# Kernel tuning notes

Measured on AMD Instinct MI355X. Metric: run time of the kernel, lower is better.

The kernel has to match this reference:

```python
import jax, jax.numpy as jnp
import numpy as np

N_HEAD, D_MODEL, D_K, D_V = 8, 128, 16, 16
EPS = 1e-5


def entmax15(x):
    # 1.5-entmax along last axis (Peters & Martins 2019, exact sort-based algo)
    x = x * 0.5
    x = x - jnp.max(x, axis=-1, keepdims=True)
    xs = jnp.flip(jnp.sort(x, axis=-1), axis=-1)  # descending
    K = x.shape[-1]
    rho = jnp.arange(1, K + 1, dtype=x.dtype)
    mean = jnp.cumsum(xs, axis=-1) / rho
    mean_sq = jnp.cumsum(xs * xs, axis=-1) / rho
    delta = (1.0 - rho * (mean_sq - mean * mean)) / rho
    tau = mean - jnp.sqrt(jnp.clip(delta, 0.0))
    support = jnp.sum(tau <= xs, axis=-1, keepdims=True)  # support size k*
    tau_star = jnp.take_along_axis(tau, support - 1, axis=-1)
    p = jnp.clip(x - tau_star, 0.0)
    return p * p


def layer_norm(x, gamma, beta):
    mu = jnp.mean(x, axis=-1, keepdims=True)
    var = jnp.mean((x - mu) ** 2, axis=-1, keepdims=True)
    return gamma * (x - mu) * jax.lax.rsqrt(var + EPS) + beta


def setup_inputs() -> dict:
    key = jax.random.key(0)
    ks = jax.random.split(key, 24)
    B, Lq, Lk, D = 4, 1024, 2048, D_MODEL
    s = 0.05
    f = jax.random.normal
    return {
        "q": f(ks[0], (B, Lq, D), jnp.float32),
        "k": f(ks[1], (B, Lk, D), jnp.float32),
        "v": f(ks[2], (B, Lk, D), jnp.float32),
        "v_2": f(ks[3], (B, Lq, D), jnp.float32),
        "W_Q": f(ks[4], (D, N_HEAD * D_K)) * s, "b_Q": f(ks[5], (N_HEAD * D_K,)) * s,
        "W_K": f(ks[6], (D, N_HEAD * D_K)) * s, "b_K": f(ks[7], (N_HEAD * D_K,)) * s,
        "W_V": f(ks[8], (D, N_HEAD * D_V)) * s, "b_V": f(ks[9], (N_HEAD * D_V,)) * s,
        "W_V2": f(ks[10], (D, N_HEAD * D_V)) * s, "b_V2": f(ks[11], (N_HEAD * D_V,)) * s,
        "W_O": f(ks[12], (N_HEAD * D_V, D)) * s, "b_O": f(ks[13], (D,)) * s,
        "W_O2": f(ks[14], (N_HEAD * D_V, D)) * s, "b_O2": f(ks[15], (D,)) * s,
        "W_R": f(ks[16], (D, D)) * s,
        "W_R2": f(ks[17], (D, D)) * s,
        "gamma": jnp.ones((D,), jnp.float32),
        "beta": jnp.zeros((D,), jnp.float32),
    }


def reference(q, k, v, v_2, W_Q, b_Q, W_K, b_K, W_V, b_V, W_V2, b_V2,
              W_O, b_O, W_O2, b_O2, W_R, W_R2, gamma, beta):
    B, Lq, _ = q.shape
    Lk = k.shape[1]
    Q = (q @ W_Q + b_Q).reshape(B, Lq, N_HEAD, D_K)
    Kh = (k @ W_K + b_K).reshape(B, Lk, N_HEAD, D_K)
    V = (v @ W_V + b_V).reshape(B, Lk, N_HEAD, D_V)
    V2 = (v_2 @ W_V2 + b_V2).reshape(B, Lq, N_HEAD, D_V)
    # scores: [B, H, Lq, Lk]
    scores = jnp.einsum('bqhd,bkhd->bhqk', Q, Kh) / np.float32(np.sqrt(D_K))
    A = entmax15(scores)                              # normalize over Lk
    A2 = entmax15(jnp.swapaxes(scores, -2, -1))       # normalize over Lq
    out = jnp.einsum('bhqk,bkhd->bqhd', A, V).reshape(B, Lq, N_HEAD * D_V)
    out2 = jnp.einsum('bhkq,bqhd->bkhd', A2, V2).reshape(B, Lk, N_HEAD * D_V)
    # dropout is identity in eval mode; both branches use the SAME layer_norm params (as in source)
    out = jax.nn.relu(layer_norm(out @ W_O + b_O + q @ W_R, gamma, beta))
    out2 = jax.nn.relu(layer_norm(out2 @ W_O2 + b_O2 + k @ W_R2, gamma, beta))
    return (out, out2, A, A2)
```

## Files before the change

### kernel.cpp

```cpp
#include <hip/hip_runtime.h>

__global__ __launch_bounds__(128) void proj_all_kernel(
    const float* __restrict__ q, const float* __restrict__ k,
    const float* __restrict__ v, const float* __restrict__ v2,
    const float* __restrict__ W_Q, const float* __restrict__ b_Q,
    const float* __restrict__ W_K, const float* __restrict__ b_K,
    const float* __restrict__ W_V, const float* __restrict__ b_V,
    const float* __restrict__ W_V2, const float* __restrict__ b_V2,
    float* __restrict__ Qp, float* __restrict__ Kp,
    float* __restrict__ Vp, float* __restrict__ V2p)
{
  __shared__ float xs[4][128];
  int blk = blockIdx.x;
  const float *X, *W, *B; float* Y; int L, chunked, rb;
  if (blk < 1024)      { X = q;  W = W_Q;  B = b_Q;  Y = Qp;  L = 1024; chunked = 1; rb = blk; }
  else if (blk < 3072) { X = k;  W = W_K;  B = b_K;  Y = Kp;  L = 2048; chunked = 1; rb = blk - 1024; }
  else if (blk < 5120) { X = v;  W = W_V;  B = b_V;  Y = Vp;  L = 2048; chunked = 0; rb = blk - 3072; }
  else                 { X = v2; W = W_V2; B = b_V2; Y = V2p; L = 1024; chunked = 0; rb = blk - 5120; }
  rb *= 4;
  int c = threadIdx.x;
#pragma unroll
  for (int i = 0; i < 4; ++i)
    xs[i][c] = X[(size_t)(rb + i) * 128 + c];
  __syncthreads();
  float b = B[c];
  float a0 = b, a1 = b, a2 = b, a3 = b;
#pragma unroll 8
  for (int d = 0; d < 128; ++d) {
    float w = W[d * 128 + c];
    a0 = fmaf(xs[0][d], w, a0);
    a1 = fmaf(xs[1][d], w, a1);
    a2 = fmaf(xs[2][d], w, a2);
    a3 = fmaf(xs[3][d], w, a3);
  }
  int h = c >> 4, dd = c & 15;
  float av[4] = { a0, a1, a2, a3 };
#pragma unroll
  for (int i = 0; i < 4; ++i) {
    int row = rb + i;
    int bb = row / L;
    int l  = row - bb * L;
    if (chunked)
      Y[(((size_t)(bb * 8 + h) * 4 + (dd >> 2)) * L + l) * 4 + (dd & 3)] = av[i];
    else
      Y[((size_t)(bb * 8 + h) * L + l) * 16 + dd] = av[i];
  }
}

static __device__ __forceinline__ float hstep(float f, float s1, float cnt)
{
  float arg = fmaf(-cnt, f, s1 * s1);
  return (arg > 0.f) ? f / (s1 + sqrtf(arg)) : f / (2.f * s1);
}

template<int LROW, int LCOL>
__global__ __launch_bounds__(256) void attn_kernel(
    const float* __restrict__ RowM, const float* __restrict__ ColM,
    const float* __restrict__ ValM, float* __restrict__ Aout,
    float* __restrict__ OutWs)
{
  constexpr int J   = LCOL / 64;
  constexpr int CAP = 512;
  constexpr float Z = 1.0f;
  __shared__ float          sval[4][CAP];
  __shared__ unsigned short sidx[4][CAP];

  int ws   = threadIdx.x >> 6;
  int wid  = blockIdx.x * 4 + ws;
  int lane = threadIdx.x & 63;
  int bh   = wid / LROW;
  int r    = wid - bh * LROW;
  int bb   = bh >> 3, h = bh & 7;

  float qf[16];
  { const float* qb = RowM + (size_t)bh * LROW * 16;
#pragma unroll
    for (int d = 0; d < 16; ++d)
      qf[d] = qb[((size_t)(d >> 2) * LROW + r) * 4 + (d & 3)] * 0.125f;
  }

  float x[J];
  const float4* Cb = (const float4*)(ColM + (size_t)bh * LCOL * 16);
#pragma unroll
  for (int j = 0; j < J; ++j) {
    int kk = lane + 64 * j;
    float4 k0 = Cb[0 * LCOL + kk];
    float  s  = qf[0] * k0.x;
    s = fmaf(qf[1], k0.y, s); s = fmaf(qf[2], k0.z, s); s = fmaf(qf[3], k0.w, s);
    float4 k1 = Cb[1 * LCOL + kk];
    s = fmaf(qf[4], k1.x, s); s = fmaf(qf[5], k1.y, s);
    s = fmaf(qf[6], k1.z, s); s = fmaf(qf[7], k1.w, s);
    float4 k2 = Cb[2 * LCOL + kk];
    s = fmaf(qf[8], k2.x, s); s = fmaf(qf[9], k2.y, s);
    s = fmaf(qf[10], k2.z, s); s = fmaf(qf[11], k2.w, s);
    float4 k3 = Cb[3 * LCOL + kk];
    s = fmaf(qf[12], k3.x, s); s = fmaf(qf[13], k3.y, s);
    s = fmaf(qf[14], k3.z, s); s = fmaf(qf[15], k3.w, s);
    x[j] = s;
  }

  float m = -1e30f, sr = 0.f, qr = 0.f;
#pragma unroll
  for (int j = 0; j < J; ++j) {
    m = fmaxf(m, x[j]);
    sr += x[j];
    qr = fmaf(x[j], x[j], qr);
  }
#pragma unroll
  for (int off = 32; off >= 1; off >>= 1) {
    m  = fmaxf(m, __shfl_xor(m, off));
    sr += __shfl_xor(sr, off);
    qr += __shfl_xor(qr, off);
  }
  float mu  = sr * (1.f / (float)LCOL);
  float sig = sqrtf(fmaxf(qr * (1.f / (float)LCOL) - mu * mu, 0.f));
  float theta = fmaxf(fmaf(Z, sig, mu), m - 1.0f);

  float* arow = Aout + ((size_t)bh * LROW + r) * LCOL;
  const float* Vb = ValM + (size_t)bh * LCOL * 16;
  float* op = OutWs + ((size_t)bb * LROW + r) * 128 + h * 16;

  int c = 0;
#pragma unroll
  for (int j = 0; j < J; ++j) c += (x[j] > theta) ? 1 : 0;
  int i = c;
#pragma unroll
  for (int off = 1; off <= 32; off <<= 1) {
    int t = __shfl_up(i, off);
    if (lane >= off) i += t;
  }
  int base = i - c;
  int tot  = __shfl(i, 63);

  if (tot >= 1 && tot <= CAP) {
    int w = 0;
#pragma unroll
    for (int j = 0; j < J; ++j) {
      if (x[j] > theta) {
        sval[ws][base + w] = x[j];
        sidx[ws][base + w] = (unsigned short)(lane + 64 * j);
        ++w;
      }
    }
    __threadfence_block();

    float tau = theta;
    bool valid = true;
    for (int it = 0; it < 24; ++it) {
      float s1 = 0.f, s2 = 0.f;
      int cnt = 0;
      for (int i2 = lane; i2 < tot; i2 += 64) {
        float t = sval[ws][i2] - tau, r0 = fmaxf(t, 0.f);
        s1 += r0; s2 = fmaf(r0, r0, s2);
        cnt += __popcll(__ballot(t > 0.f));
      }
#pragma unroll
      for (int off = 32; off >= 1; off >>= 1) {
        s1 += __shfl_xor(s1, off);
        s2 += __shfl_xor(s2, off);
      }
      float f = s2 - 1.0f;
      if (it == 0 && f < -1e-6f) { valid = false; break; }
      if (f > 1e-6f && s1 > 1e-12f) tau += hstep(f, s1, (float)cnt);
      else break;
    }

    if (valid) {
#pragma unroll
      for (int j = 0; j < J; ++j) {
        int kk = lane + 64 * j;
        float t = fmaxf(x[j] - tau, 0.f);
        __builtin_nontemporal_store(t * t, &arow[kk]);
      }

      float acc[16];
#pragma unroll
      for (int d = 0; d < 16; ++d) acc[d] = 0.f;
      for (int i2 = lane; i2 < tot; i2 += 64) {
        float t = sval[ws][i2] - tau;
        if (t > 0.f) {
          float p = t * t;
          int kk = sidx[ws][i2];
          const float4* vp = (const float4*)(Vb + (size_t)kk * 16);
          float4 v0 = vp[0], v1 = vp[1], v2 = vp[2], v3 = vp[3];
          acc[0]  = fmaf(p, v0.x, acc[0]);  acc[1]  = fmaf(p, v0.y, acc[1]);
          acc[2]  = fmaf(p, v0.z, acc[2]);  acc[3]  = fmaf(p, v0.w, acc[3]);
          acc[4]  = fmaf(p, v1.x, acc[4]);  acc[5]  = fmaf(p, v1.y, acc[5]);
          acc[6]  = fmaf(p, v1.z, acc[6]);  acc[7]  = fmaf(p, v1.w, acc[7]);
          acc[8]  = fmaf(p, v2.x, acc[8]);  acc[9]  = fmaf(p, v2.y, acc[9]);
          acc[10] = fmaf(p, v2.z, acc[10]); acc[11] = fmaf(p, v2.w, acc[11]);
          acc[12] = fmaf(p, v3.x, acc[12]); acc[13] = fmaf(p, v3.y, acc[13]);
          acc[14] = fmaf(p, v3.z, acc[14]); acc[15] = fmaf(p, v3.w, acc[15]);
        }
      }
#pragma unroll
      for (int off = 32; off >= 1; off >>= 1)
#pragma unroll
        for (int d = 0; d < 16; ++d) acc[d] += __shfl_xor(acc[d], off);
      float vv = acc[0];
#pragma unroll
      for (int d = 1; d < 16; ++d)
        vv = (lane == d) ? acc[d] : vv;
      if (lane < 16) op[lane] = vv;
      return;
    }
  }

  float tau = m - 1.0f;
  bool done = false;
  for (int it = 0; it < 24; ++it) {
    float a1 = 0.f, a2 = 0.f;
    int ac = 0;
#pragma unroll
    for (int j = 0; j < J; ++j) {
      float t = x[j] - tau, r0 = fmaxf(t, 0.f);
      a1 += r0; a2 = fmaf(r0, r0, a2);
      ac += __popcll(__ballot(t > 0.f));
    }
#pragma unroll
    for (int off = 32; off >= 1; off >>= 1) {
      a1 += __shfl_xor(a1, off);
      a2 += __shfl_xor(a2, off);
    }
    float f = a2 - 1.0f;
    bool g = !done && (f > 1e-6f) && (a1 > 1e-12f);
    if (g) tau += hstep(f, a1, (float)ac); else done = true;
    if (done) break;
  }

  float acc[16];
#pragma unroll
  for (int d = 0; d < 16; ++d) acc[d] = 0.f;
#pragma unroll
  for (int j = 0; j < J; ++j) {
    int kk = lane + 64 * j;
    float t = fmaxf(x[j] - tau, 0.f), p = t * t;
    __builtin_nontemporal_store(p, &arow[kk]);
    const float4* vp = (const float4*)(Vb + (size_t)kk * 16);
    float4 v0 = vp[0], v1 = vp[1], v2 = vp[2], v3 = vp[3];
    acc[0]  = fmaf(p, v0.x, acc[0]);  acc[1]  = fmaf(p, v0.y, acc[1]);
    acc[2]  = fmaf(p, v0.z, acc[2]);  acc[3]  = fmaf(p, v0.w, acc[3]);
    acc[4]  = fmaf(p, v1.x, acc[4]);  acc[5]  = fmaf(p, v1.y, acc[5]);
    acc[6]  = fmaf(p, v1.z, acc[6]);  acc[7]  = fmaf(p, v1.w, acc[7]);
    acc[8]  = fmaf(p, v2.x, acc[8]);  acc[9]  = fmaf(p, v2.y, acc[9]);
    acc[10] = fmaf(p, v2.z, acc[10]); acc[11] = fmaf(p, v2.w, acc[11]);
    acc[12] = fmaf(p, v3.x, acc[12]); acc[13] = fmaf(p, v3.y, acc[13]);
    acc[14] = fmaf(p, v3.z, acc[14]); acc[15] = fmaf(p, v3.w, acc[15]);
  }
#pragma unroll
  for (int off = 32; off >= 1; off >>= 1)
#pragma unroll
    for (int d = 0; d < 16; ++d) acc[d] += __shfl_xor(acc[d], off);
  float vv = acc[0];
#pragma unroll
  for (int d = 1; d < 16; ++d)
    vv = (lane == d) ? acc[d] : vv;
  if (lane < 16) op[lane] = vv;
}

__global__ __launch_bounds__(128) void combine_ln_kernel(
    const float* __restrict__ X1, const float* __restrict__ X2,
    const float* __restrict__ W1, const float* __restrict__ W2,
    const float* __restrict__ bias, const float* __restrict__ gamma,
    const float* __restrict__ beta, float* __restrict__ O)
{
  __shared__ float x1s[4][128], x2s[4][128];
  __shared__ float red[2][8];
  int rb = blockIdx.x * 4;
  int c  = threadIdx.x;
#pragma unroll
  for (int i = 0; i < 4; ++i) {
    x1s[i][c] = X1[(size_t)(rb + i) * 128 + c];
    x2s[i][c] = X2[(size_t)(rb + i) * 128 + c];
  }
  __syncthreads();
  float b = bias[c];
  float a0 = b, a1 = b, a2 = b, a3 = b;
#pragma unroll 8
  for (int d = 0; d < 128; ++d) {
    float w1 = W1[d * 128 + c];
    float w2 = W2[d * 128 + c];
    a0 = fmaf(x1s[0][d], w1, fmaf(x2s[0][d], w2, a0));
    a1 = fmaf(x1s[1][d], w1, fmaf(x2s[1][d], w2, a1));
    a2 = fmaf(x1s[2][d], w1, fmaf(x2s[2][d], w2, a2));
    a3 = fmaf(x1s[3][d], w1, fmaf(x2s[3][d], w2, a3));
  }
  float s0 = a0, s1 = a1, s2 = a2, s3 = a3;
  float q0 = a0 * a0, q1 = a1 * a1, q2 = a2 * a2, q3 = a3 * a3;
#pragma unroll
  for (int off = 32; off >= 1; off >>= 1) {
    s0 += __shfl_xor(s0, off); q0 += __shfl_xor(q0, off);
    s1 += __shfl_xor(s1, off); q1 += __shfl_xor(q1, off);
    s2 += __shfl_xor(s2, off); q2 += __shfl_xor(q2, off);
    s3 += __shfl_xor(s3, off); q3 += __shfl_xor(q3, off);
  }
  int wv = c >> 6;
  if ((c & 63) == 0) {
    red[wv][0] = s0; red[wv][1] = q0; red[wv][2] = s1; red[wv][3] = q1;
    red[wv][4] = s2; red[wv][5] = q2; red[wv][6] = s3; red[wv][7] = q3;
  }
  __syncthreads();
  float S0 = red[0][0] + red[1][0], Q0 = red[0][1] + red[1][1];
  float S1 = red[0][2] + red[1][2], Q1 = red[0][3] + red[1][3];
  float S2 = red[0][4] + red[1][4], Q2 = red[0][5] + red[1][5];
  float S3 = red[0][6] + red[1][6], Q3 = red[0][7] + red[1][7];
  float g = gamma[c], be = beta[c];
  float mu, var, rs;
  mu = S0 * (1.f / 128.f); var = fmaxf(Q0 * (1.f / 128.f) - mu * mu, 0.f);
  rs = rsqrtf(var + 1e-5f);
  O[(size_t)(rb + 0) * 128 + c] = fmaxf(fmaf((a0 - mu) * rs, g, be), 0.f);
  mu = S1 * (1.f / 128.f); var = fmaxf(Q1 * (1.f / 128.f) - mu * mu, 0.f);
  rs = rsqrtf(var + 1e-5f);
  O[(size_t)(rb + 1) * 128 + c] = fmaxf(fmaf((a1 - mu) * rs, g, be), 0.f);
  mu = S2 * (1.f / 128.f); var = fmaxf(Q2 * (1.f / 128.f) - mu * mu, 0.f);
  rs = rsqrtf(var + 1e-5f);
  O[(size_t)(rb + 2) * 128 + c] = fmaxf(fmaf((a2 - mu) * rs, g, be), 0.f);
  mu = S3 * (1.f / 128.f); var = fmaxf(Q3 * (1.f / 128.f) - mu * mu, 0.f);
  rs = rsqrtf(var + 1e-5f);
  O[(size_t)(rb + 3) * 128 + c] = fmaxf(fmaf((a3 - mu) * rs, g, be), 0.f);
}

extern "C"
__attribute__((visibility("default"), used))
void kernel_launch(void* const* d_in, const int* in_sizes, int n_in,
                   void* d_out, int out_size, void* d_ws, size_t ws_size,
                   hipStream_t stream)
{
  (void)in_sizes; (void)n_in; (void)out_size; (void)ws_size;
  const float* q     = (const float*)d_in[0];
  const float* k     = (const float*)d_in[1];
  const float* v     = (const float*)d_in[2];
  const float* v2    = (const float*)d_in[3];
  const float* W_Q   = (const float*)d_in[4];
  const float* b_Q   = (const float*)d_in[5];
  const float* W_K   = (const float*)d_in[6];
  const float* b_K   = (const float*)d_in[7];
  const float* W_V   = (const float*)d_in[8];
  const float* b_V   = (const float*)d_in[9];
  const float* W_V2  = (const float*)d_in[10];
  const float* b_V2  = (const float*)d_in[11];
  const float* W_O   = (const float*)d_in[12];
  const float* b_O   = (const float*)d_in[13];
  const float* W_O2  = (const float*)d_in[14];
  const float* b_O2  = (const float*)d_in[15];
  const float* W_R   = (const float*)d_in[16];
  const float* W_R2  = (const float*)d_in[17];
  const float* gamma = (const float*)d_in[18];
  const float* beta  = (const float*)d_in[19];

  char* ws = (char*)d_ws;
  const size_t MB = 1u << 20;
  float* Qp    = (float*)(ws + 0);
  float* Kp    = (float*)(ws + 2 * MB);
  float* Vp    = (float*)(ws + 6 * MB);
  float* V2p   = (float*)(ws + 10 * MB);
  float* outm1 = (float*)(ws + 12 * MB);
  float* outm2 = (float*)(ws + 14 * MB);

  float* out1  = (float*)d_out;
  float* out2  = out1 + (size_t)524288;
  float* Aout  = out1 + (size_t)1572864;
  float* A2out = out1 + (size_t)68681728;

  proj_all_kernel<<<6144, 128, 0, stream>>>(
      q, k, v, v2, W_Q, b_Q, W_K, b_K, W_V, b_V, W_V2, b_V2,
      Qp, Kp, Vp, V2p);

  attn_kernel<1024, 2048><<<8192,  256, 0, stream>>>(Qp, Kp, Vp,  Aout,  outm1);
  attn_kernel<2048, 1024><<<16384, 256, 0, stream>>>(Kp, Qp, V2p, A2out, outm2);

  combine_ln_kernel<<<1024, 128, 0, stream>>>(outm1, q, W_O,  W_R,  b_O,
                                              gamma, beta, out1);
  combine_ln_kernel<<<2048, 128, 0, stream>>>(outm2, k, W_O2, W_R2, b_O2,
                                              gamma, beta, out2);
}
```

Before: 1.061 ms.

## Split each attention row across two wavefronts with shared-memory stat exchange

Each attention row is now handled by two wavefronts, each covering half the columns. Partial max, sum and sum-of-squares statistics and support counts are combined through shared memory, and the scores are staged in LDS for the fallback path. The goal is to halve per-wave register use so occupancy rises and more work is in flight. The cost is block-level syncs, a larger LDS footprint per block, and serial PV accumulation on only one wave per row, so the other wave sits idle during that step.

New measurement: 1.179 ms. 1.11x slower.

```diff
diff --git a/kernel.cpp b/kernel.cpp
--- a/kernel.cpp
+++ b/kernel.cpp
@@ -54,23 +54,30 @@
 }
 
 template<int LROW, int LCOL>
-__global__ __launch_bounds__(256) void attn_kernel(
+__global__ __launch_bounds__(256) void attn_split_kernel(
     const float* __restrict__ RowM, const float* __restrict__ ColM,
     const float* __restrict__ ValM, float* __restrict__ Aout,
     float* __restrict__ OutWs)
 {
-  constexpr int J   = LCOL / 64;
+  constexpr int JH  = LCOL / 128;
   constexpr int CAP = 512;
   constexpr float Z = 1.0f;
-  __shared__ float          sval[4][CAP];
-  __shared__ unsigned short sidx[4][CAP];
-
-  int ws   = threadIdx.x >> 6;
-  int wid  = blockIdx.x * 4 + ws;
-  int lane = threadIdx.x & 63;
-  int bh   = wid / LROW;
-  int r    = wid - bh * LROW;
-  int bb   = bh >> 3, h = bh & 7;
+
+  __shared__ float          xbuf[2][LCOL];
+  __shared__ float          sval[2][CAP];
+  __shared__ unsigned short sidx[2][CAP];
+  __shared__ float          stats[2][2][3];
+  __shared__ int            tots[2][2];
+
+  int ws      = threadIdx.x >> 6;
+  int rowslot = ws >> 1;
+  int half    = ws & 1;
+  int lane    = threadIdx.x & 63;
+  int wid     = blockIdx.x * 2 + rowslot;
+  int bh      = wid / LROW;
+  int r       = wid - bh * LROW;
+  int bb      = bh >> 3, h = bh & 7;
+  int colbase = half * (LCOL / 2);
 
   float qf[16];
   { const float* qb = RowM + (size_t)bh * LROW * 16;
@@ -79,11 +86,11 @@
       qf[d] = qb[((size_t)(d >> 2) * LROW + r) * 4 + (d & 3)] * 0.125f;
   }
 
-  float x[J];
+  float x[JH];
   const float4* Cb = (const float4*)(ColM + (size_t)bh * LCOL * 16);
 #pragma unroll
-  for (int j = 0; j < J; ++j) {
-    int kk = lane + 64 * j;
+  for (int j = 0; j < JH; ++j) {
+    int kk = colbase + lane + 64 * j;
     float4 k0 = Cb[0 * LCOL + kk];
     float  s  = qf[0] * k0.x;
     s = fmaf(qf[1], k0.y, s); s = fmaf(qf[2], k0.z, s); s = fmaf(qf[3], k0.w, s);
@@ -97,21 +104,31 @@
     s = fmaf(qf[12], k3.x, s); s = fmaf(qf[13], k3.y, s);
     s = fmaf(qf[14], k3.z, s); s = fmaf(qf[15], k3.w, s);
     x[j] = s;
-  }
-
-  float m = -1e30f, sr = 0.f, qr = 0.f;
-#pragma unroll
-  for (int j = 0; j < J; ++j) {
-    m = fmaxf(m, x[j]);
-    sr += x[j];
-    qr = fmaf(x[j], x[j], qr);
+    xbuf[rowslot][kk] = s;
+  }
+
+  float ml = -1e30f, sl = 0.f, ql = 0.f;
+#pragma unroll
+  for (int j = 0; j < JH; ++j) {
+    ml = fmaxf(ml, x[j]);
+    sl += x[j];
+    ql = fmaf(x[j], x[j], ql);
   }
 #pragma unroll
   for (int off = 32; off >= 1; off >>= 1) {
-    m  = fmaxf(m, __shfl_xor(m, off));
-    sr += __shfl_xor(sr, off);
-    qr += __shfl_xor(qr, off);
-  }
+    ml = fmaxf(ml, __shfl_xor(ml, off));
+    sl += __shfl_xor(sl, off);
+    ql += __shfl_xor(ql, off);
+  }
+  if (lane == 0) {
+    stats[rowslot][half][0] = ml;
+    stats[rowslot][half][1] = sl;
+    stats[rowslot][half][2] = ql;
+  }
+  __syncthreads();
+  float m  = fmaxf(stats[rowslot][0][0], stats[rowslot][1][0]);
+  float sr = stats[rowslot][0][1] + stats[rowslot][1][1];
+  float qr = stats[rowslot][0][2] + stats[rowslot][1][2];
   float mu  = sr * (1.f / (float)LCOL);
   float sig = sqrtf(fmaxf(qr * (1.f / (float)LCOL) - mu * mu, 0.f));
   float theta = fmaxf(fmaf(Z, sig, mu), m - 1.0f);
@@ -122,35 +139,43 @@
 
   int c = 0;
 #pragma unroll
-  for (int j = 0; j < J; ++j) c += (x[j] > theta) ? 1 : 0;
-  int i = c;
+  for (int j = 0; j < JH; ++j) c += (x[j] > theta) ? 1 : 0;
+  int pre = c;
 #pragma unroll
   for (int off = 1; off <= 32; off <<= 1) {
-    int t = __shfl_up(i, off);
-    if (lane >= off) i += t;
-  }
-  int base = i - c;
-  int tot  = __shfl(i, 63);
-
-  if (tot >= 1 && tot <= CAP) {
+    int t = __shfl_up(pre, off);
+    if (lane >= off) pre += t;
+  }
+  int totH = __shfl(pre, 63);
+  if (lane == 0) tots[rowslot][half] = totH;
+  __syncthreads();
+  int tot0 = tots[rowslot][0];
+  int tot  = tot0 + tots[rowslot][1];
+  int base = (pre - c) + (half ? tot0 : 0);
+
+  bool fastok = (tot >= 1 && tot <= CAP);
+  if (fastok) {
     int w = 0;
 #pragma unroll
-    for (int j = 0; j < J; ++j) {
+    for (int j = 0; j < JH; ++j) {
       if (x[j] > theta) {
-        sval[ws][base + w] = x[j];
-        sidx[ws][base + w] = (unsigned short)(lane + 64 * j);
+        sval[rowslot][base + w] = x[j];
+        sidx[rowslot][base + w] = (unsigned short)(colbase + lane + 64 * j);
         ++w;
       }
     }
-    __threadfence_block();
-
+  }
+  __threadfence_block();
+  __syncthreads();
+
+  if (fastok) {
     float tau = theta;
     bool valid = true;
     for (int it = 0; it < 24; ++it) {
       float s1 = 0.f, s2 = 0.f;
       int cnt = 0;
       for (int i2 = lane; i2 < tot; i2 += 64) {
-        float t = sval[ws][i2] - tau, r0 = fmaxf(t, 0.f);
+        float t = sval[rowslot][i2] - tau, r0 = fmaxf(t, 0.f);
         s1 += r0; s2 = fmaf(r0, r0, s2);
         cnt += __popcll(__ballot(t > 0.f));
       }
@@ -167,41 +192,42 @@
 
     if (valid) {
 #pragma unroll
-      for (int j = 0; j < J; ++j) {
-        int kk = lane + 64 * j;
+      for (int j = 0; j < JH; ++j) {
+        int kk = colbase + lane + 64 * j;
         float t = fmaxf(x[j] - tau, 0.f);
         __builtin_nontemporal_store(t * t, &arow[kk]);
       }
-
-      float acc[16];
-#pragma unroll
-      for (int d = 0; d < 16; ++d) acc[d] = 0.f;
-      for (int i2 = lane; i2 < tot; i2 += 64) {
-        float t = sval[ws][i2] - tau;
-        if (t > 0.f) {
-          float p = t * t;
-          int kk = sidx[ws][i2];
-          const float4* vp = (const float4*)(Vb + (size_t)kk * 16);
-          float4 v0 = vp[0], v1 = vp[1], v2 = vp[2], v3 = vp[3];
-          acc[0]  = fmaf(p, v0.x, acc[0]);  acc[1]  = fmaf(p, v0.y, acc[1]);
-          acc[2]  = fmaf(p, v0.z, acc[2]);  acc[3]  = fmaf(p, v0.w, acc[3]);
-          acc[4]  = fmaf(p, v1.x, acc[4]);  acc[5]  = fmaf(p, v1.y, acc[5]);
-          acc[6]  = fmaf(p, v1.z, acc[6]);  acc[7]  = fmaf(p, v1.w, acc[7]);
-          acc[8]  = fmaf(p, v2.x, acc[8]);  acc[9]  = fmaf(p, v2.y, acc[9]);
-          acc[10] = fmaf(p, v2.z, acc[10]); acc[11] = fmaf(p, v2.w, acc[11]);
-          acc[12] = fmaf(p, v3.x, acc[12]); acc[13] = fmaf(p, v3.y, acc[13]);
-          acc[14] = fmaf(p, v3.z, acc[14]); acc[15] = fmaf(p, v3.w, acc[15]);
+      if (half == 0) {
+        float acc[16];
+#pragma unroll
+        for (int d = 0; d < 16; ++d) acc[d] = 0.f;
+        for (int i2 = lane; i2 < tot; i2 += 64) {
+          float t = sval[rowslot][i2] - tau;
+          if (t > 0.f) {
+            float p = t * t;
+            int kk = sidx[rowslot][i2];
+            const float4* vp = (const float4*)(Vb + (size_t)kk * 16);
+            float4 v0 = vp[0], v1 = vp[1], v2 = vp[2], v3 = vp[3];
+            acc[0]  = fmaf(p, v0.x, acc[0]);  acc[1]  = fmaf(p, v0.y, acc[1]);
+            acc[2]  = fmaf(p, v0.z, acc[2]);  acc[3]  = fmaf(p, v0.w, acc[3]);
+            acc[4]  = fmaf(p, v1.x, acc[4]);  acc[5]  = fmaf(p, v1.y, acc[5]);
+            acc[6]  = fmaf(p, v1.z, acc[6]);  acc[7]  = fmaf(p, v1.w, acc[7]);
+            acc[8]  = fmaf(p, v2.x, acc[8]);  acc[9]  = fmaf(p, v2.y, acc[9]);
+            acc[10] = fmaf(p, v2.z, acc[10]); acc[11] = fmaf(p, v2.w, acc[11]);
+            acc[12] = fmaf(p, v3.x, acc[12]); acc[13] = fmaf(p, v3.y, acc[13]);
+            acc[14] = fmaf(p, v3.z, acc[14]); acc[15] = fmaf(p, v3.w, acc[15]);
+          }
         }
-      }
-#pragma unroll
-      for (int off = 32; off >= 1; off >>= 1)
-#pragma unroll
-        for (int d = 0; d < 16; ++d) acc[d] += __shfl_xor(acc[d], off);
-      float vv = acc[0];
-#pragma unroll
-      for (int d = 1; d < 16; ++d)
-        vv = (lane == d) ? acc[d] : vv;
-      if (lane < 16) op[lane] = vv;
+#pragma unroll
+        for (int off = 32; off >= 1; off >>= 1)
+#pragma unroll
+          for (int d = 0; d < 16; ++d) acc[d] += __shfl_xor(acc[d], off);
+        float vv = acc[0];
+#pragma unroll
+        for (int d = 1; d < 16; ++d)
+          vv = (lane == d) ? acc[d] : vv;
+        if (lane < 16) op[lane] = vv;
+      }
       return;
     }
   }
@@ -211,9 +237,8 @@
   for (int it = 0; it < 24; ++it) {
     float a1 = 0.f, a2 = 0.f;
     int ac = 0;
-#pragma unroll
-    for (int j = 0; j < J; ++j) {
-      float t = x[j] - tau, r0 = fmaxf(t, 0.f);
+    for (int i = lane; i < LCOL; i += 64) {
+      float t = xbuf[rowslot][i] - tau, r0 = fmaxf(t, 0.f);
       a1 += r0; a2 = fmaf(r0, r0, a2);
       ac += __popcll(__ballot(t > 0.f));
     }
@@ -228,34 +253,42 @@
     if (done) break;
   }
 
-  float acc[16];
-#pragma unroll
-  for (int d = 0; d < 16; ++d) acc[d] = 0.f;
-#pragma unroll
-  for (int j = 0; j < J; ++j) {
-    int kk = lane + 64 * j;
-    float t = fmaxf(x[j] - tau, 0.f), p = t * t;
-    __builtin_nontemporal_store(p, &arow[kk]);
-    const float4* vp = (const float4*)(Vb + (size_t)kk * 16);
-    float4 v0 = vp[0], v1 = vp[1], v2 = vp[2], v3 = vp[3];
-    acc[0]  = fmaf(p, v0.x, acc[0]);  acc[1]  = fmaf(p, v0.y, acc[1]);
-    acc[2]  = fmaf(p, v0.z, acc[2]);  acc[3]  = fmaf(p, v0.w, acc[3]);
-    acc[4]  = fmaf(p, v1.x, acc[4]);  acc[5]  = fmaf(p, v1.y, acc[5]);
-    acc[6]  = fmaf(p, v1.z, acc[6]);  acc[7]  = fmaf(p, v1.w, acc[7]);
-    acc[8]  = fmaf(p, v2.x, acc[8]);  acc[9]  = fmaf(p, v2.y, acc[9]);
-    acc[10] = fmaf(p, v2.z, acc[10]); acc[11] = fmaf(p, v2.w, acc[11]);
-    acc[12] = fmaf(p, v3.x, acc[12]); acc[13] = fmaf(p, v3.y, acc[13]);
-    acc[14] = fmaf(p, v3.z, acc[14]); acc[15] = fmaf(p, v3.w, acc[15]);
-  }
-#pragma unroll
-  for (int off = 32; off >= 1; off >>= 1)
-#pragma unroll
-    for (int d = 0; d < 16; ++d) acc[d] += __shfl_xor(acc[d], off);
-  float vv = acc[0];
-#pragma unroll
-  for (int d = 1; d < 16; ++d)
-    vv = (lane == d) ? acc[d] : vv;
-  if (lane < 16) op[lane] = vv;
+#pragma unroll
+  for (int j = 0; j < JH; ++j) {
+    int kk = colbase + lane + 64 * j;
+    float t = fmaxf(x[j] - tau, 0.f);
+    __builtin_nontemporal_store(t * t, &arow[kk]);
+  }
+  if (half == 0) {
+    float acc[16];
+#pragma unroll
+    for (int d = 0; d < 16; ++d) acc[d] = 0.f;
+    for (int i = lane; i < LCOL; i += 64) {
+      float t = fmaxf(xbuf[rowslot][i] - tau, 0.f);
+      if (t > 0.f) {
+        float p = t * t;
+        const float4* vp = (const float4*)(Vb + (size_t)i * 16);
+        float4 v0 = vp[0], v1 = vp[1], v2 = vp[2], v3 = vp[3];
+        acc[0]  = fmaf(p, v0.x, acc[0]);  acc[1]  = fmaf(p, v0.y, acc[1]);
+        acc[2]  = fmaf(p, v0.z, acc[2]);  acc[3]  = fmaf(p, v0.w, acc[3]);
+        acc[4]  = fmaf(p, v1.x, acc[4]);  acc[5]  = fmaf(p, v1.y, acc[5]);
+        acc[6]  = fmaf(p, v1.z, acc[6]);  acc[7]  = fmaf(p, v1.w, acc[7]);
+        acc[8]  = fmaf(p, v2.x, acc[8]);  acc[9]  = fmaf(p, v2.y, acc[9]);
+        acc[10] = fmaf(p, v2.z, acc[10]); acc[11] = fmaf(p, v2.w, acc[11]);
+        acc[12] = fmaf(p, v3.x, acc[12]); acc[13] = fmaf(p, v3.y, acc[13]);
+        acc[14] = fmaf(p, v3.z, acc[14]); acc[15] = fmaf(p, v3.w, acc[15]);
+      }
+    }
+#pragma unroll
+    for (int off = 32; off >= 1; off >>= 1)
+#pragma unroll
+      for (int d = 0; d < 16; ++d) acc[d] += __shfl_xor(acc[d], off);
+    float vv = acc[0];
+#pragma unroll
+    for (int d = 1; d < 16; ++d)
+      vv = (lane == d) ? acc[d] : vv;
+    if (lane < 16) op[lane] = vv;
+  }
 }
 
 __global__ __launch_bounds__(128) void combine_ln_kernel(
@@ -366,8 +399,10 @@
       q, k, v, v2, W_Q, b_Q, W_K, b_K, W_V, b_V, W_V2, b_V2,
       Qp, Kp, Vp, V2p);
 
-  attn_kernel<1024, 2048><<<8192,  256, 0, stream>>>(Qp, Kp, Vp,  Aout,  outm1);
-  attn_kernel<2048, 1024><<<16384, 256, 0, stream>>>(Kp, Qp, V2p, A2out, outm2);
+  attn_split_kernel<1024, 2048><<<16384, 256, 0, stream>>>(
+      Qp, Kp, Vp, Aout, outm1);
+  attn_split_kernel<2048, 1024><<<32768, 256, 0, stream>>>(
+      Kp, Qp, V2p, A2out, outm2);
 
   combine_ln_kernel<<<1024, 128, 0, stream>>>(outm1, q, W_O,  W_R,  b_O,
                                               gamma, beta, out1);
```
